# Performance work log

Hardware: AMD Instinct MI355X
Metric: run time of the kernel (lower is better)

## Reference

```python
import jax, jax.numpy as jnp
import numpy as np

DIM = 512
NUM_HEAD = 8
HEAD_DIM = DIM // NUM_HEAD
FFN = 4 * DIM


def setup_inputs() -> dict:
    key = jax.random.key(0)
    ks = jax.random.split(key, 16)
    s = DIM ** -0.5
    inp = {
        "x": jax.random.normal(ks[0], (4, 2048, DIM), jnp.float32),
        "wq": jax.random.normal(ks[1], (DIM, DIM), jnp.float32) * s,
        "bq": jnp.zeros((DIM,), jnp.float32),
        "wk": jax.random.normal(ks[2], (DIM, DIM), jnp.float32) * s,
        "bk": jnp.zeros((DIM,), jnp.float32),
        "wv": jax.random.normal(ks[3], (DIM, DIM), jnp.float32) * s,
        "bv": jnp.zeros((DIM,), jnp.float32),
        "wo": jax.random.normal(ks[4], (DIM, DIM), jnp.float32) * s,
        "bo": jnp.zeros((DIM,), jnp.float32),
        "w1": jax.random.normal(ks[5], (DIM, FFN), jnp.float32) * s,
        "b1": jnp.zeros((FFN,), jnp.float32),
        "w2": jax.random.normal(ks[6], (FFN, DIM), jnp.float32) * (FFN ** -0.5),
        "b2": jnp.zeros((DIM,), jnp.float32),
        "g1": jnp.ones((DIM,), jnp.float32),
        "be1": jnp.zeros((DIM,), jnp.float32),
        "g2": jnp.ones((DIM,), jnp.float32),
        "be2": jnp.zeros((DIM,), jnp.float32),
    }
    return inp


def layer_norm(x, g, b, eps=1e-5):
    mu = jnp.mean(x, axis=-1, keepdims=True)
    var = jnp.var(x, axis=-1, keepdims=True)
    return (x - mu) * jax.lax.rsqrt(var + eps) * g + b


def _forward(x, wq, bq, wk, bk, wv, bv, wo, bo, w1, b1, w2, b2, g1, be1, g2, be2):
    b, n, _ = x.shape
    scale = HEAD_DIM ** -0.5
    q = (x @ wq + bq).reshape(b, n, NUM_HEAD, HEAD_DIM).transpose(0, 2, 1, 3)
    k = (x @ wk + bk).reshape(b, n, NUM_HEAD, HEAD_DIM).transpose(0, 2, 1, 3)
    v = (x @ wv + bv).reshape(b, n, NUM_HEAD, HEAD_DIM).transpose(0, 2, 1, 3)
    scores = jnp.einsum('bhqd,bhkd->bhqk', q, k) * scale
    attn = jax.nn.softmax(scores, axis=-1)
    out = jnp.einsum('bhqk,bhkd->bhqd', attn, v)
    out = out.transpose(0, 2, 1, 3).reshape(b, n, DIM)
    out = out @ wo + bo
    x = layer_norm(out + x, g1, be1)
    h = jax.nn.gelu(x @ w1 + b1, approximate=False)
    ff = h @ w2 + b2
    x = layer_norm(ff + x, g2, be2)
    return x


def reference(x, wq, bq, wk, bk, wv, bv, wo, bo, w1, b1, w2, b2, g1, be1, g2, be2):
    return _forward(x, wq, bq, wk, bk, wv, bv, wo, bo, w1, b1, w2, b2, g1, be1, g2, be2)
```

## Files before the change

### kernel.cpp

```cpp
#include <hip/hip_runtime.h>
#include <math.h>

#define DIM 512
#define NHEAD 8
#define HD 64
#define FFN_DIM 2048
#define BATCH 4
#define SEQ 2048
#define MTOK (BATCH*SEQ)

typedef __attribute__((ext_vector_type(8))) short bf16x8;
typedef __attribute__((ext_vector_type(4))) short bf16x4;
typedef __attribute__((ext_vector_type(4))) float f32x4;
typedef __attribute__((ext_vector_type(2))) unsigned int u32x2;
typedef __attribute__((ext_vector_type(4))) unsigned int u32x4;

__device__ __forceinline__ unsigned short f2b(float f){
    unsigned int u = __float_as_uint(f);
    u += 0x7fffu + ((u >> 16) & 1u);
    return (unsigned short)(u >> 16);
}
__device__ __forceinline__ float b2f(unsigned short u){
    return __uint_as_float(((unsigned int)u) << 16);
}
__device__ __forceinline__ unsigned int pack_trunc(float f0, float f1){
    return __builtin_amdgcn_perm(__float_as_uint(f1), __float_as_uint(f0), 0x07060302u);
}
__device__ __forceinline__ void async_cp16(const unsigned short* g, unsigned short* l){
    __builtin_amdgcn_global_load_lds((const __attribute__((address_space(1))) unsigned int*)g,
                                     (__attribute__((address_space(3))) unsigned int*)l, 16, 0, 0);
}
__device__ __forceinline__ float gelu_fast(float x){
    float x3 = x*x*x;
    float y  = 2.302588f * (x + 0.044715f*x3);
    float t  = __builtin_amdgcn_exp2f(y);
    return x * t * __builtin_amdgcn_rcpf(t + 1.0f);
}

__device__ __forceinline__ void transp32(const float* __restrict__ in, unsigned short* __restrict__ out,
                                         int N, int K, int n0_rd, int n0_wr, int k0,
                                         unsigned short (&t)[32][33], int tid){
    int tx = tid & 31, ty = tid >> 5;
    #pragma unroll
    for (int u = 0; u < 4; u++)
        t[tx][ty + 8*u] = f2b(in[(size_t)(k0 + ty + 8*u)*N + n0_rd + tx]);
    __syncthreads();
    #pragma unroll
    for (int u = 0; u < 4; u++)
        out[(size_t)(n0_wr + ty + 8*u)*K + k0 + tx] = t[ty + 8*u][tx];
}

__global__ void prep_kernel(const float* __restrict__ x,
                            const float* __restrict__ wq, const float* __restrict__ wk,
                            const float* __restrict__ wv, const float* __restrict__ wo,
                            const float* __restrict__ w1, const float* __restrict__ w2,
                            const float* __restrict__ bq, const float* __restrict__ bk,
                            const float* __restrict__ bv,
                            unsigned short* __restrict__ xb, unsigned short* __restrict__ wqkvT,
                            unsigned short* __restrict__ woT, unsigned short* __restrict__ w1T,
                            unsigned short* __restrict__ w2T, float* __restrict__ bqkv)
{
    __shared__ unsigned short t[32][33];
    int bid = blockIdx.x, tid = threadIdx.x;
    if (bid < 4096) {
        int i = (bid*256 + tid)*4;
        float4 v = *(const float4*)(x + i);
        ushort4 o; o.x=f2b(v.x); o.y=f2b(v.y); o.z=f2b(v.z); o.w=f2b(v.w);
        *(ushort4*)(xb + i) = o;
    } else if (bid < 4864) {
        int r = bid - 4096;
        int n0 = (r % 48)*32, k0 = (r / 48)*32;
        const float* w = (n0 < 512) ? wq : (n0 < 1024) ? wk : wv;
        transp32(w, wqkvT, 512, 512, n0 & 511, n0, k0, t, tid);
    } else if (bid < 5120) {
        int r = bid - 4864;
        int n0 = (r % 16)*32, k0 = (r / 16)*32;
        transp32(wo, woT, 512, 512, n0, n0, k0, t, tid);
    } else if (bid < 6144) {
        int r = bid - 5120;
        int n0 = (r % 64)*32, k0 = (r / 64)*32;
        transp32(w1, w1T, 2048, 512, n0, n0, k0, t, tid);
    } else if (bid < 7168) {
        int r = bid - 6144;
        int n0 = (r % 16)*32, k0 = (r / 16)*32;
        transp32(w2, w2T, 512, 2048, n0, n0, k0, t, tid);
    } else {
        int i = (bid - 7168)*256 + tid;
        if (i < 1536)
            bqkv[i] = (i < 512) ? bq[i] : (i < 1024) ? bk[i-512] : bv[i-1024];
    }
}

template<int MODE, int SK>
__global__ __launch_bounds__(512, 4)
void gemm_bf16(const unsigned short* __restrict__ A, const unsigned short* __restrict__ Bt,
               const float* __restrict__ bias,
               unsigned short* __restrict__ Cb,
               unsigned short* __restrict__ qo, unsigned short* __restrict__ ko,
               unsigned short* __restrict__ vTo,
               int M, int N, int K)
{
    __shared__ unsigned short lds[36864];
    int tid  = threadIdx.x;
    int lane = tid & 63;
    int ln = lane & 15, qd = lane >> 4;
    int m0 = blockIdx.x * 256, n0 = blockIdx.y * 128;
    int wid = tid >> 6;
    int wm = (wid >> 1) * 64;
    int wn = (wid & 1) * 64;
    int kbeg = (SK > 1) ? (int)blockIdx.z * (K/SK) : 0;
    int nk = (K/SK) >> 5;
    if (SK > 1 && MODE == 0) Cb += (size_t)blockIdx.z * M * N;

    f32x4 acc[4][4];
    #pragma unroll
    for (int i = 0; i < 4; i++)
        #pragma unroll
        for (int j = 0; j < 4; j++) acc[i][j] = (f32x4){0.f,0.f,0.f,0.f};

#define G_STAGE(K0_, BUF_)                                                              \
    {                                                                                   \
        _Pragma("unroll")                                                               \
        for (int i = 0; i < 2; i++) {                                                   \
            int cid = i*512 + tid;                                                      \
            int row = cid >> 2, cs = cid & 3;                                           \
            int cg = cs ^ ((row >> 1) & 3);                                             \
            async_cp16(&A[(size_t)(m0+row)*K + (K0_) + cg*8], &lds[(BUF_) + (cid & ~63) * 8]); \
        }                                                                               \
        {                                                                               \
            int cid = tid;                                                              \
            int row = cid >> 2, cs = cid & 3;                                           \
            int cg = cs ^ ((row >> 1) & 3);                                             \
            async_cp16(&Bt[(size_t)(n0+row)*K + (K0_) + cg*8], &lds[(BUF_) + 8192 + (cid & ~63) * 8]); \
        }                                                                               \
    }

    G_STAGE(kbeg,      0)
    G_STAGE(kbeg + 32, 12288)

    int swz = (qd ^ ((ln >> 1) & 3)) * 8;
    int aoff = (wm + ln)*32 + swz;
    int boff = 8192 + (wn + ln)*32 + swz;

    int kof = 0;
    for (int t = 0; t < nk; t++) {
        if (t < nk - 1) { asm volatile("s_waitcnt vmcnt(3)" ::: "memory"); }
        else            { asm volatile("s_waitcnt vmcnt(0)" ::: "memory"); }
        __builtin_amdgcn_s_barrier();
        __builtin_amdgcn_sched_barrier(0);
        if (t < nk - 2) {
            int nb = kof + 24576; if (nb >= 36864) nb -= 36864;
            G_STAGE(kbeg + (t+2)*32, nb)
        }
        bf16x8 af[4], bf[4];
        #pragma unroll
        for (int tt = 0; tt < 4; tt++) {
            af[tt] = *(bf16x8*)&lds[kof + aoff + tt*512];
            bf[tt] = *(bf16x8*)&lds[kof + boff + tt*512];
        }
        __builtin_amdgcn_s_setprio(1);
        #pragma unroll
        for (int i = 0; i < 4; i++)
            #pragma unroll
            for (int j = 0; j < 4; j++)
                acc[i][j] = __builtin_amdgcn_mfma_f32_16x16x32_bf16(af[i], bf[j], acc[i][j], 0,0,0);
        __builtin_amdgcn_s_setprio(0);
        kof += 12288; if (kof >= 36864) kof = 0;
    }
#undef G_STAGE

    const float QSCALE = 0.18033688011112042f;
    #pragma unroll
    for (int i = 0; i < 4; i++) {
        int mb = m0 + wm + i*16 + qd*4;
        #pragma unroll
        for (int j = 0; j < 4; j++) {
            int c = n0 + wn + j*16 + ln;
            float bv_ = (SK > 1 && blockIdx.z) ? 0.f : bias[c];
            float v[4];
            #pragma unroll
            for (int r = 0; r < 4; r++) v[r] = acc[i][j][r] + bv_;
            if (MODE == 0) {
                #pragma unroll
                for (int r = 0; r < 4; r++) Cb[(size_t)(mb+r)*N + c] = f2b(v[r]);
            } else if (MODE == 2) {
                #pragma unroll
                for (int r = 0; r < 4; r++)
                    Cb[(size_t)(mb+r)*N + c] = f2b(gelu_fast(v[r]));
            } else {
                int b = mb >> 11, t0 = mb & 2047;
                if (c < 512) {
                    int h = c >> 6, hd = c & 63;
                    #pragma unroll
                    for (int r = 0; r < 4; r++)
                        qo[(((size_t)(b*8 + h))*SEQ + t0 + r)*64 + hd] = f2b(v[r] * QSCALE);
                } else if (c < 1024) {
                    int cc = c - 512, h = cc >> 6, hd = cc & 63;
                    #pragma unroll
                    for (int r = 0; r < 4; r++)
                        ko[(((size_t)(b*8 + h))*SEQ + t0 + r)*64 + hd] = f2b(v[r]);
                } else {
                    int cc = c - 1024, h = cc >> 6, hd = cc & 63;
                    ushort4 pk;
                    pk.x = f2b(v[0]); pk.y = f2b(v[1]); pk.z = f2b(v[2]); pk.w = f2b(v[3]);
                    *(ushort4*)&vTo[(((size_t)(b*8 + h))*64 + hd)*SEQ + t0] = pk;
                }
            }
        }
    }
}

#define ATTN_BODY(KT_, KOF_, PREF_, VMC_)                                               \
  {                                                                                     \
    asm volatile("s_waitcnt vmcnt(" #VMC_ ")" ::: "memory");                            \
    __builtin_amdgcn_s_barrier();                                                       \
    __builtin_amdgcn_sched_barrier(0);                                                  \
    if (PREF_) {                                                                        \
      const int nb = (KOF_ + 16384) % 24576;                                            \
      async_cp16(&K [((size_t)bh*SEQ + ((KT_)+2)*64 + srow)*64 + scg*8], &lds[nb + sdst]); \
      async_cp16(&VT[((size_t)bh*64 + srow)*SEQ + ((KT_)+2)*64 + scg*8], &lds[nb + 4096 + sdst]); \
    }                                                                                   \
    bf16x8 kf[2][2];                                                                    \
    _Pragma("unroll")                                                                   \
    for (int ntl = 0; ntl < 2; ntl++) {                                                 \
      kf[ntl][0] = *(const bf16x8*)&kp0[(KOF_) + ntl*1024];                             \
      kf[ntl][1] = *(const bf16x8*)&kp1[(KOF_) + ntl*1024];                             \
    }                                                                                   \
    f32x4 s[2][2];                                                                      \
    _Pragma("unroll")                                                                   \
    for (int qs = 0; qs < 2; qs++)                                                      \
      _Pragma("unroll")                                                                 \
      for (int ntl = 0; ntl < 2; ntl++) s[qs][ntl] = (f32x4){0.f,0.f,0.f,0.f};          \
    __builtin_amdgcn_s_setprio(1);                                                      \
    _Pragma("unroll")                                                                   \
    for (int kk = 0; kk < 2; kk++) {                                                    \
      _Pragma("unroll")                                                                 \
      for (int ntl = 0; ntl < 2; ntl++) {                                               \
        s[0][ntl] = __builtin_amdgcn_mfma_f32_16x16x32_bf16(kf[ntl][kk], qf[0][kk], s[0][ntl], 0,0,0); \
        s[1][ntl] = __builtin_amdgcn_mfma_f32_16x16x32_bf16(kf[ntl][kk], qf[1][kk], s[1][ntl], 0,0,0); \
      }                                                                                 \
    }                                                                                   \
    __builtin_amdgcn_s_setprio(0);                                                      \
    bf16x8 pf[2];                                                                       \
    _Pragma("unroll")                                                                   \
    for (int qs = 0; qs < 2; qs++) {                                                    \
      float p[8];                                                                       \
      _Pragma("unroll")                                                                 \
      for (int ntl = 0; ntl < 2; ntl++)                                                 \
        _Pragma("unroll")                                                               \
        for (int r = 0; r < 4; r++) p[ntl*4+r] = __builtin_amdgcn_exp2f(s[qs][ntl][r]); \
      l_i[qs] += ((p[0]+p[1])+(p[2]+p[3])) + ((p[4]+p[5])+(p[6]+p[7]));                 \
      u32x4 pu;                                                                         \
      pu[0] = pack_trunc(p[0], p[1]); pu[1] = pack_trunc(p[2], p[3]);                   \
      pu[2] = pack_trunc(p[4], p[5]); pu[3] = pack_trunc(p[6], p[7]);                   \
      pf[qs] = __builtin_bit_cast(bf16x8, pu);                                          \
    }                                                                                   \
    __builtin_amdgcn_s_setprio(1);                                                      \
    _Pragma("unroll")                                                                   \
    for (int dt = 0; dt < 4; dt++) {                                                    \
      u32x2 va = *(const u32x2*)&vpA[(KOF_) + 4096 + dt*1024];                          \
      u32x2 vb = *(const u32x2*)&vpB[(KOF_) + 4096 + dt*1024];                          \
      u32x4 vv; vv[0] = va[0]; vv[1] = va[1]; vv[2] = vb[0]; vv[3] = vb[1];             \
      bf16x8 vf = __builtin_bit_cast(bf16x8, vv);                                       \
      o[0][dt] = __builtin_amdgcn_mfma_f32_16x16x32_bf16(vf, pf[0], o[0][dt], 0,0,0);   \
      o[1][dt] = __builtin_amdgcn_mfma_f32_16x16x32_bf16(vf, pf[1], o[1][dt], 0,0,0);   \
    }                                                                                   \
    __builtin_amdgcn_s_setprio(0);                                                      \
  }

__global__ __launch_bounds__(512, 2)
void attn_mfma(const unsigned short* __restrict__ Q, const unsigned short* __restrict__ K,
               const unsigned short* __restrict__ VT, unsigned short* __restrict__ O)
{
    __shared__ unsigned short lds[24576];
    int tid  = threadIdx.x;
    int wid  = tid >> 6, lane = tid & 63;
    int ln = lane & 15, qd = lane >> 4;
    int wq = wid & 3;
    int wk = wid >> 2;
    int bx = blockIdx.x;
    int qb = (bx >> 3) & 15;
    int bh = (bx & 7) + 8 * (bx >> 7);

    bf16x8 qf[2][2];
    #pragma unroll
    for (int qs = 0; qs < 2; qs++)
        #pragma unroll
        for (int kk = 0; kk < 2; kk++)
            qf[qs][kk] = *(const bf16x8*)&Q[((size_t)bh*SEQ + qb*128 + wq*32 + qs*16 + ln)*64 + kk*32 + qd*8];

    int srow = tid >> 3, scs = tid & 7, scg = scs ^ (srow & 7);
    int sdst = (tid & ~63) * 8;
    #pragma unroll
    for (int t = 0; t < 2; t++) {
        async_cp16(&K [((size_t)bh*SEQ + t*64 + srow)*64 + scg*8], &lds[t*8192 + sdst]);
        async_cp16(&VT[((size_t)bh*64 + srow)*SEQ + t*64 + scg*8], &lds[t*8192 + 4096 + sdst]);
    }

    const unsigned short* kp0 = lds + wk*2048 + ln*64 + ((0*4 + qd) ^ (ln & 7))*8;
    const unsigned short* kp1 = lds + wk*2048 + ln*64 + ((1*4 + qd) ^ (ln & 7))*8;
    const unsigned short* vpA = lds + ln*64 + ((wk*4     + (qd>>1)) ^ (ln & 7))*8 + (qd & 1)*4;
    const unsigned short* vpB = lds + ln*64 + ((wk*4 + 2 + (qd>>1)) ^ (ln & 7))*8 + (qd & 1)*4;

    f32x4 o[2][4];
    #pragma unroll
    for (int qs = 0; qs < 2; qs++)
        #pragma unroll
        for (int dt = 0; dt < 4; dt++) o[qs][dt] = (f32x4){0.f,0.f,0.f,0.f};
    float l_i[2] = {0.f, 0.f};

    for (int kt3 = 0; kt3 < 30; kt3 += 3) {
        ATTN_BODY(kt3 + 0, 0,     true, 2)
        ATTN_BODY(kt3 + 1, 8192,  true, 2)
        ATTN_BODY(kt3 + 2, 16384, true, 2)
    }
    ATTN_BODY(30, 0,    false, 2)
    ATTN_BODY(31, 8192, false, 0)

    float l[2];
    #pragma unroll
    for (int qs = 0; qs < 2; qs++) {
        float t = l_i[qs];
        t += __shfl_xor(t, 16);
        t += __shfl_xor(t, 32);
        l[qs] = t;
    }

    __syncthreads();
    float* fl = (float*)lds;
    if (wk == 1) {
        #pragma unroll
        for (int qs = 0; qs < 2; qs++) {
            #pragma unroll
            for (int dt = 0; dt < 4; dt++)
                *(f32x4*)&fl[(((wq*2 + qs)*4 + dt)*64 + lane)*4] = o[qs][dt];
            fl[8192 + (wq*2 + qs)*64 + lane] = l[qs];
        }
    }
    __syncthreads();
    if (wk == 0) {
        int b = bh >> 3, h = bh & 7;
        #pragma unroll
        for (int qs = 0; qs < 2; qs++) {
            float lt = l[qs] + fl[8192 + (wq*2 + qs)*64 + lane];
            float linv = 1.0f / lt;
            int t = qb*128 + wq*32 + qs*16 + ln;
            #pragma unroll
            for (int dt = 0; dt < 4; dt++) {
                f32x4 po = *(f32x4*)&fl[(((wq*2 + qs)*4 + dt)*64 + lane)*4];
                ushort4 pk;
                pk.x = f2b((o[qs][dt][0] + po[0])*linv);
                pk.y = f2b((o[qs][dt][1] + po[1])*linv);
                pk.z = f2b((o[qs][dt][2] + po[2])*linv);
                pk.w = f2b((o[qs][dt][3] + po[3])*linv);
                *(ushort4*)&O[((size_t)b*SEQ + t)*DIM + h*64 + dt*16 + qd*4] = pk;
            }
        }
    }
}

__global__ void ln1_kernel(const unsigned short* __restrict__ m0b, const unsigned short* __restrict__ m1b,
                           const float* __restrict__ resp,
                           const float* __restrict__ g, const float* __restrict__ be,
                           unsigned short* __restrict__ outb)
{
    int row  = blockIdx.x*4 + (threadIdx.x >> 6);
    int lane = threadIdx.x & 63;
    size_t base = (size_t)row * DIM + lane*8;

    ushort4 a0 = *(const ushort4*)(m0b + base);
    ushort4 a1 = *(const ushort4*)(m0b + base + 4);
    ushort4 c0 = *(const ushort4*)(m1b + base);
    ushort4 c1 = *(const ushort4*)(m1b + base + 4);
    float4 r0 = *(const float4*)(resp + base);
    float4 r1 = *(const float4*)(resp + base + 4);
    float v[8] = { b2f(a0.x)+b2f(c0.x)+r0.x, b2f(a0.y)+b2f(c0.y)+r0.y,
                   b2f(a0.z)+b2f(c0.z)+r0.z, b2f(a0.w)+b2f(c0.w)+r0.w,
                   b2f(a1.x)+b2f(c1.x)+r1.x, b2f(a1.y)+b2f(c1.y)+r1.y,
                   b2f(a1.z)+b2f(c1.z)+r1.z, b2f(a1.w)+b2f(c1.w)+r1.w };
    float s = 0.f, s2 = 0.f;
    #pragma unroll
    for (int i = 0; i < 8; i++) { s += v[i]; s2 += v[i]*v[i]; }
    #pragma unroll
    for (int d = 32; d >= 1; d >>= 1) { s += __shfl_xor(s, d); s2 += __shfl_xor(s2, d); }
    float mean = s * (1.0f / DIM);
    float rstd = rsqrtf(s2 * (1.0f / DIM) - mean*mean + 1e-5f);

    float4 g0 = *(const float4*)(g + lane*8);
    float4 g1 = *(const float4*)(g + lane*8 + 4);
    float4 b0 = *(const float4*)(be + lane*8);
    float4 b1 = *(const float4*)(be + lane*8 + 4);
    float gg[8] = {g0.x,g0.y,g0.z,g0.w,g1.x,g1.y,g1.z,g1.w};
    float bb[8] = {b0.x,b0.y,b0.z,b0.w,b1.x,b1.y,b1.z,b1.w};
    float o[8];
    #pragma unroll
    for (int i = 0; i < 8; i++) o[i] = (v[i]-mean)*rstd*gg[i] + bb[i];
    ushort4 p0, p1;
    p0.x=f2b(o[0]); p0.y=f2b(o[1]); p0.z=f2b(o[2]); p0.w=f2b(o[3]);
    p1.x=f2b(o[4]); p1.y=f2b(o[5]); p1.z=f2b(o[6]); p1.w=f2b(o[7]);
    *(ushort4*)(outb + base)     = p0;
    *(ushort4*)(outb + base + 4) = p1;
}

__global__ void ln2_kernel(const unsigned short* __restrict__ m0b, const unsigned short* __restrict__ m1b,
                           const unsigned short* __restrict__ resb,
                           const float* __restrict__ g, const float* __restrict__ be,
                           float* __restrict__ outf)
{
    int row  = blockIdx.x*4 + (threadIdx.x >> 6);
    int lane = threadIdx.x & 63;
    size_t base = (size_t)row * DIM + lane*8;

    ushort4 a0 = *(const ushort4*)(m0b + base);
    ushort4 a1 = *(const ushort4*)(m0b + base + 4);
    ushort4 c0 = *(const ushort4*)(m1b + base);
    ushort4 c1 = *(const ushort4*)(m1b + base + 4);
    ushort4 rb0 = *(const ushort4*)(resb + base);
    ushort4 rb1 = *(const ushort4*)(resb + base + 4);
    float v[8] = { b2f(a0.x)+b2f(c0.x)+b2f(rb0.x), b2f(a0.y)+b2f(c0.y)+b2f(rb0.y),
                   b2f(a0.z)+b2f(c0.z)+b2f(rb0.z), b2f(a0.w)+b2f(c0.w)+b2f(rb0.w),
                   b2f(a1.x)+b2f(c1.x)+b2f(rb1.x), b2f(a1.y)+b2f(c1.y)+b2f(rb1.y),
                   b2f(a1.z)+b2f(c1.z)+b2f(rb1.z), b2f(a1.w)+b2f(c1.w)+b2f(rb1.w) };
    float s = 0.f, s2 = 0.f;
    #pragma unroll
    for (int i = 0; i < 8; i++) { s += v[i]; s2 += v[i]*v[i]; }
    #pragma unroll
    for (int d = 32; d >= 1; d >>= 1) { s += __shfl_xor(s, d); s2 += __shfl_xor(s2, d); }
    float mean = s * (1.0f / DIM);
    float rstd = rsqrtf(s2 * (1.0f / DIM) - mean*mean + 1e-5f);

    float4 g0 = *(const float4*)(g + lane*8);
    float4 g1 = *(const float4*)(g + lane*8 + 4);
    float4 b0 = *(const float4*)(be + lane*8);
    float4 b1 = *(const float4*)(be + lane*8 + 4);
    float gg[8] = {g0.x,g0.y,g0.z,g0.w,g1.x,g1.y,g1.z,g1.w};
    float bb[8] = {b0.x,b0.y,b0.z,b0.w,b1.x,b1.y,b1.z,b1.w};
    float o[8];
    #pragma unroll
    for (int i = 0; i < 8; i++) o[i] = (v[i] - mean)*rstd*gg[i] + bb[i];
    *(float4*)(outf + base)     = (float4){o[0],o[1],o[2],o[3]};
    *(float4*)(outf + base + 4) = (float4){o[4],o[5],o[6],o[7]};
}

extern "C" void kernel_launch(void* const* d_in, const int* in_sizes, int n_in,
                              void* d_out, int out_size, void* d_ws, size_t ws_size,
                              hipStream_t stream) {
    const float* x   = (const float*)d_in[0];
    const float* wq  = (const float*)d_in[1];
    const float* bq  = (const float*)d_in[2];
    const float* wk  = (const float*)d_in[3];
    const float* bk  = (const float*)d_in[4];
    const float* wv  = (const float*)d_in[5];
    const float* bv  = (const float*)d_in[6];
    const float* wo  = (const float*)d_in[7];
    const float* bo  = (const float*)d_in[8];
    const float* w1  = (const float*)d_in[9];
    const float* b1  = (const float*)d_in[10];
    const float* w2  = (const float*)d_in[11];
    const float* b2  = (const float*)d_in[12];
    const float* g1  = (const float*)d_in[13];
    const float* be1 = (const float*)d_in[14];
    const float* g2  = (const float*)d_in[15];
    const float* be2 = (const float*)d_in[16];
    float* out = (float*)d_out;

    char* w = (char*)d_ws;
    size_t off = 0;
    auto alloc = [&](size_t bytes){ void* p = w + off; off += (bytes + 255) & ~(size_t)255; return p; };
    unsigned short* xb     = (unsigned short*)alloc((size_t)MTOK*DIM*2);
    unsigned short* wqkvT  = (unsigned short*)alloc((size_t)1536*512*2);
    unsigned short* woT    = (unsigned short*)alloc((size_t)512*512*2);
    unsigned short* w1T    = (unsigned short*)alloc((size_t)2048*512*2);
    unsigned short* w2T    = (unsigned short*)alloc((size_t)512*2048*2);
    float*          bqkv   = (float*)alloc(1536*4);
    unsigned short* qb_    = (unsigned short*)alloc((size_t)32*SEQ*64*2);
    unsigned short* kb_    = (unsigned short*)alloc((size_t)32*SEQ*64*2);
    unsigned short* vT_    = (unsigned short*)alloc((size_t)32*64*SEQ*2);
    unsigned short* attno  = (unsigned short*)alloc((size_t)MTOK*DIM*2);
    unsigned short* x1b    = (unsigned short*)alloc((size_t)MTOK*DIM*2);
    unsigned short* h_     = (unsigned short*)alloc((size_t)MTOK*FFN_DIM*2);
    unsigned short* ffb    = (unsigned short*)alloc((size_t)2*MTOK*DIM*2);

    prep_kernel<<<7174, 256, 0, stream>>>(x, wq, wk, wv, wo, w1, w2, bq, bk, bv,
                                          xb, wqkvT, woT, w1T, w2T, bqkv);

    gemm_bf16<1,1><<<dim3(32,12), 512, 0, stream>>>(xb, wqkvT, bqkv, nullptr,
                                                    qb_, kb_, vT_, MTOK, 1536, DIM);
    attn_mfma<<<512, 512, 0, stream>>>(qb_, kb_, vT_, attno);
    gemm_bf16<0,2><<<dim3(32,4,2), 512, 0, stream>>>(attno, woT, bo, ffb,
                                                     nullptr, nullptr, nullptr, MTOK, DIM, DIM);
    ln1_kernel<<<MTOK/4, 256, 0, stream>>>(ffb, ffb + (size_t)MTOK*DIM, x, g1, be1, x1b);
    gemm_bf16<2,1><<<dim3(32,16), 512, 0, stream>>>(x1b, w1T, b1, h_,
                                                    nullptr, nullptr, nullptr, MTOK, FFN_DIM, DIM);
    gemm_bf16<0,2><<<dim3(32,4,2), 512, 0, stream>>>(h_, w2T, b2, ffb,
                                                     nullptr, nullptr, nullptr, MTOK, DIM, FFN_DIM);
    ln2_kernel<<<MTOK/4, 256, 0, stream>>>(ffb, ffb + (size_t)MTOK*DIM, x1b, g2, be2, out);
}
```

Before: 238.9 us.

## Software-pipeline attention QK^T one tile ahead with 4-stage LDS ring

Restructures the attention inner loop so that each iteration computes QK^T scores for the next key tile while it runs exp/PV on the current tile, ping-ponging between two score register sets. The K/V shared-memory ring grows from three to four 8K-element stages with prefetch distance three, so loads are issued further ahead. This aims to overlap MFMA latency of the two matmuls and hide global-load latency. In exchange it uses more registers and more LDS per block, which may reduce occupancy at the requested launch bounds of 2 blocks.

```diff
diff --git a/kernel.cpp b/kernel.cpp
--- a/kernel.cpp
+++ b/kernel.cpp
@@ -210,37 +210,37 @@
     }
 }
 
-#define ATTN_BODY(KT_, KOF_, PREF_, VMC_)                                               \
+#define ATTN_ITER(T_, VBUF_, K1BUF_, PBUF_, PREF_, VMC_, SC_, SN_, DOQK_)               \
   {                                                                                     \
     asm volatile("s_waitcnt vmcnt(" #VMC_ ")" ::: "memory");                            \
     __builtin_amdgcn_s_barrier();                                                       \
     __builtin_amdgcn_sched_barrier(0);                                                  \
     if (PREF_) {                                                                        \
-      const int nb = (KOF_ + 16384) % 24576;                                            \
-      async_cp16(&K [((size_t)bh*SEQ + ((KT_)+2)*64 + srow)*64 + scg*8], &lds[nb + sdst]); \
-      async_cp16(&VT[((size_t)bh*64 + srow)*SEQ + ((KT_)+2)*64 + scg*8], &lds[nb + 4096 + sdst]); \
+      async_cp16(&K [((size_t)bh*SEQ + ((T_)+3)*64 + srow)*64 + scg*8], &lds[(PBUF_) + sdst]); \
+      async_cp16(&VT[((size_t)bh*64 + srow)*SEQ + ((T_)+3)*64 + scg*8], &lds[(PBUF_) + 4096 + sdst]); \
     }                                                                                   \
-    bf16x8 kf[2][2];                                                                    \
-    _Pragma("unroll")                                                                   \
-    for (int ntl = 0; ntl < 2; ntl++) {                                                 \
-      kf[ntl][0] = *(const bf16x8*)&kp0[(KOF_) + ntl*1024];                             \
-      kf[ntl][1] = *(const bf16x8*)&kp1[(KOF_) + ntl*1024];                             \
-    }                                                                                   \
-    f32x4 s[2][2];                                                                      \
-    _Pragma("unroll")                                                                   \
-    for (int qs = 0; qs < 2; qs++)                                                      \
-      _Pragma("unroll")                                                                 \
-      for (int ntl = 0; ntl < 2; ntl++) s[qs][ntl] = (f32x4){0.f,0.f,0.f,0.f};          \
-    __builtin_amdgcn_s_setprio(1);                                                      \
-    _Pragma("unroll")                                                                   \
-    for (int kk = 0; kk < 2; kk++) {                                                    \
+    if (DOQK_) {                                                                        \
+      bf16x8 kf[2][2];                                                                  \
       _Pragma("unroll")                                                                 \
       for (int ntl = 0; ntl < 2; ntl++) {                                               \
-        s[0][ntl] = __builtin_amdgcn_mfma_f32_16x16x32_bf16(kf[ntl][kk], qf[0][kk], s[0][ntl], 0,0,0); \
-        s[1][ntl] = __builtin_amdgcn_mfma_f32_16x16x32_bf16(kf[ntl][kk], qf[1][kk], s[1][ntl], 0,0,0); \
+        kf[ntl][0] = *(const bf16x8*)&kp0[(K1BUF_) + ntl*1024];                         \
+        kf[ntl][1] = *(const bf16x8*)&kp1[(K1BUF_) + ntl*1024];                         \
       }                                                                                 \
+      _Pragma("unroll")                                                                 \
+      for (int qs = 0; qs < 2; qs++)                                                    \
+        _Pragma("unroll")                                                               \
+        for (int ntl = 0; ntl < 2; ntl++) SN_[qs][ntl] = (f32x4){0.f,0.f,0.f,0.f};      \
+      __builtin_amdgcn_s_setprio(1);                                                    \
+      _Pragma("unroll")                                                                 \
+      for (int kk = 0; kk < 2; kk++) {                                                  \
+        _Pragma("unroll")                                                               \
+        for (int ntl = 0; ntl < 2; ntl++) {                                             \
+          SN_[0][ntl] = __builtin_amdgcn_mfma_f32_16x16x32_bf16(kf[ntl][kk], qf[0][kk], SN_[0][ntl], 0,0,0); \
+          SN_[1][ntl] = __builtin_amdgcn_mfma_f32_16x16x32_bf16(kf[ntl][kk], qf[1][kk], SN_[1][ntl], 0,0,0); \
+        }                                                                               \
+      }                                                                                 \
+      __builtin_amdgcn_s_setprio(0);                                                    \
     }                                                                                   \
-    __builtin_amdgcn_s_setprio(0);                                                      \
     bf16x8 pf[2];                                                                       \
     _Pragma("unroll")                                                                   \
     for (int qs = 0; qs < 2; qs++) {                                                    \
@@ -248,7 +248,7 @@
       _Pragma("unroll")                                                                 \
       for (int ntl = 0; ntl < 2; ntl++)                                                 \
         _Pragma("unroll")                                                               \
-        for (int r = 0; r < 4; r++) p[ntl*4+r] = __builtin_amdgcn_exp2f(s[qs][ntl][r]); \
+        for (int r = 0; r < 4; r++) p[ntl*4+r] = __builtin_amdgcn_exp2f(SC_[qs][ntl][r]); \
       l_i[qs] += ((p[0]+p[1])+(p[2]+p[3])) + ((p[4]+p[5])+(p[6]+p[7]));                 \
       u32x4 pu;                                                                         \
       pu[0] = pack_trunc(p[0], p[1]); pu[1] = pack_trunc(p[2], p[3]);                   \
@@ -258,8 +258,8 @@
     __builtin_amdgcn_s_setprio(1);                                                      \
     _Pragma("unroll")                                                                   \
     for (int dt = 0; dt < 4; dt++) {                                                    \
-      u32x2 va = *(const u32x2*)&vpA[(KOF_) + 4096 + dt*1024];                          \
-      u32x2 vb = *(const u32x2*)&vpB[(KOF_) + 4096 + dt*1024];                          \
+      u32x2 va = *(const u32x2*)&vpA[(VBUF_) + 4096 + dt*1024];                         \
+      u32x2 vb = *(const u32x2*)&vpB[(VBUF_) + 4096 + dt*1024];                         \
       u32x4 vv; vv[0] = va[0]; vv[1] = va[1]; vv[2] = vb[0]; vv[3] = vb[1];             \
       bf16x8 vf = __builtin_bit_cast(bf16x8, vv);                                       \
       o[0][dt] = __builtin_amdgcn_mfma_f32_16x16x32_bf16(vf, pf[0], o[0][dt], 0,0,0);   \
@@ -272,7 +272,7 @@
 void attn_mfma(const unsigned short* __restrict__ Q, const unsigned short* __restrict__ K,
                const unsigned short* __restrict__ VT, unsigned short* __restrict__ O)
 {
-    __shared__ unsigned short lds[24576];
+    __shared__ unsigned short lds[32768];
     int tid  = threadIdx.x;
     int wid  = tid >> 6, lane = tid & 63;
     int ln = lane & 15, qd = lane >> 4;
@@ -292,7 +292,7 @@
     int srow = tid >> 3, scs = tid & 7, scg = scs ^ (srow & 7);
     int sdst = (tid & ~63) * 8;
     #pragma unroll
-    for (int t = 0; t < 2; t++) {
+    for (int t = 0; t < 3; t++) {
         async_cp16(&K [((size_t)bh*SEQ + t*64 + srow)*64 + scg*8], &lds[t*8192 + sdst]);
         async_cp16(&VT[((size_t)bh*64 + srow)*SEQ + t*64 + scg*8], &lds[t*8192 + 4096 + sdst]);
     }
@@ -308,14 +308,42 @@
         #pragma unroll
         for (int dt = 0; dt < 4; dt++) o[qs][dt] = (f32x4){0.f,0.f,0.f,0.f};
     float l_i[2] = {0.f, 0.f};
-
-    for (int kt3 = 0; kt3 < 30; kt3 += 3) {
-        ATTN_BODY(kt3 + 0, 0,     true, 2)
-        ATTN_BODY(kt3 + 1, 8192,  true, 2)
-        ATTN_BODY(kt3 + 2, 16384, true, 2)
-    }
-    ATTN_BODY(30, 0,    false, 2)
-    ATTN_BODY(31, 8192, false, 0)
+    f32x4 sA[2][2], sB[2][2];
+
+    asm volatile("s_waitcnt vmcnt(4)" ::: "memory");
+    __builtin_amdgcn_s_barrier();
+    __builtin_amdgcn_sched_barrier(0);
+    {
+        bf16x8 kf[2][2];
+        #pragma unroll
+        for (int ntl = 0; ntl < 2; ntl++) {
+            kf[ntl][0] = *(const bf16x8*)&kp0[ntl*1024];
+            kf[ntl][1] = *(const bf16x8*)&kp1[ntl*1024];
+        }
+        #pragma unroll
+        for (int qs = 0; qs < 2; qs++)
+            #pragma unroll
+            for (int ntl = 0; ntl < 2; ntl++) sA[qs][ntl] = (f32x4){0.f,0.f,0.f,0.f};
+        #pragma unroll
+        for (int kk = 0; kk < 2; kk++) {
+            #pragma unroll
+            for (int ntl = 0; ntl < 2; ntl++) {
+                sA[0][ntl] = __builtin_amdgcn_mfma_f32_16x16x32_bf16(kf[ntl][kk], qf[0][kk], sA[0][ntl], 0,0,0);
+                sA[1][ntl] = __builtin_amdgcn_mfma_f32_16x16x32_bf16(kf[ntl][kk], qf[1][kk], sA[1][ntl], 0,0,0);
+            }
+        }
+    }
+
+    for (int t4 = 0; t4 < 28; t4 += 4) {
+        ATTN_ITER(t4+0, 0,     8192,  24576, true, 2, sA, sB, true)
+        ATTN_ITER(t4+1, 8192,  16384, 0,     true, 2, sB, sA, true)
+        ATTN_ITER(t4+2, 16384, 24576, 8192,  true, 2, sA, sB, true)
+        ATTN_ITER(t4+3, 24576, 0,     16384, true, 2, sB, sA, true)
+    }
+    ATTN_ITER(28, 0,     8192,  24576, true,  2, sA, sB, true)
+    ATTN_ITER(29, 8192,  16384, 0,     false, 2, sB, sA, true)
+    ATTN_ITER(30, 16384, 24576, 0,     false, 0, sA, sB, true)
+    ATTN_ITER(31, 24576, 0,     0,     false, 0, sB, sA, false)
 
     float l[2];
     #pragma unroll
```

Measured after the change: 240.7 us. No clear change (+0.8%).

## Split attention over two key halves and merge partials in a combine kernel

Applied to the files above, without the earlier changes.

The attention grid gains a second dimension, so each block processes only half of the key sequence (16 tiles instead of 32). Each block writes unnormalized partial outputs in bf16 plus per-row softmax denominators. A new combine kernel adds the two partials and divides by the summed denominators. This doubles the block count to raise parallelism and shorten each block's serial key loop. In exchange it adds a second launch, extra global traffic for the partial outputs, a duplicated pipeline prologue per block, and rounding of unnormalized partials to bf16.

```diff
diff --git a/kernel.cpp b/kernel.cpp
--- a/kernel.cpp
+++ b/kernel.cpp
@@ -217,8 +217,8 @@
     __builtin_amdgcn_sched_barrier(0);                                                  \
     if (PREF_) {                                                                        \
       const int nb = (KOF_ + 16384) % 24576;                                            \
-      async_cp16(&K [((size_t)bh*SEQ + ((KT_)+2)*64 + srow)*64 + scg*8], &lds[nb + sdst]); \
-      async_cp16(&VT[((size_t)bh*64 + srow)*SEQ + ((KT_)+2)*64 + scg*8], &lds[nb + 4096 + sdst]); \
+      async_cp16(&K [((size_t)bh*SEQ + (kzo+(KT_)+2)*64 + srow)*64 + scg*8], &lds[nb + sdst]); \
+      async_cp16(&VT[((size_t)bh*64 + srow)*SEQ + (kzo+(KT_)+2)*64 + scg*8], &lds[nb + 4096 + sdst]); \
     }                                                                                   \
     bf16x8 kf[2][2];                                                                    \
     _Pragma("unroll")                                                                   \
@@ -270,7 +270,9 @@
 
 __global__ __launch_bounds__(512, 2)
 void attn_mfma(const unsigned short* __restrict__ Q, const unsigned short* __restrict__ K,
-               const unsigned short* __restrict__ VT, unsigned short* __restrict__ O)
+               const unsigned short* __restrict__ VT,
+               unsigned short* __restrict__ O0, unsigned short* __restrict__ O1,
+               float* __restrict__ LP)
 {
     __shared__ unsigned short lds[24576];
     int tid  = threadIdx.x;
@@ -281,6 +283,8 @@
     int bx = blockIdx.x;
     int qb = (bx >> 3) & 15;
     int bh = (bx & 7) + 8 * (bx >> 7);
+    int kz = blockIdx.y;
+    int kzo = kz << 4;
 
     bf16x8 qf[2][2];
     #pragma unroll
@@ -293,8 +297,8 @@
     int sdst = (tid & ~63) * 8;
     #pragma unroll
     for (int t = 0; t < 2; t++) {
-        async_cp16(&K [((size_t)bh*SEQ + t*64 + srow)*64 + scg*8], &lds[t*8192 + sdst]);
-        async_cp16(&VT[((size_t)bh*64 + srow)*SEQ + t*64 + scg*8], &lds[t*8192 + 4096 + sdst]);
+        async_cp16(&K [((size_t)bh*SEQ + (kzo+t)*64 + srow)*64 + scg*8], &lds[t*8192 + sdst]);
+        async_cp16(&VT[((size_t)bh*64 + srow)*SEQ + (kzo+t)*64 + scg*8], &lds[t*8192 + 4096 + sdst]);
     }
 
     const unsigned short* kp0 = lds + wk*2048 + ln*64 + ((0*4 + qd) ^ (ln & 7))*8;
@@ -309,13 +313,15 @@
         for (int dt = 0; dt < 4; dt++) o[qs][dt] = (f32x4){0.f,0.f,0.f,0.f};
     float l_i[2] = {0.f, 0.f};
 
-    for (int kt3 = 0; kt3 < 30; kt3 += 3) {
+    for (int kt3 = 0; kt3 < 12; kt3 += 3) {
         ATTN_BODY(kt3 + 0, 0,     true, 2)
         ATTN_BODY(kt3 + 1, 8192,  true, 2)
         ATTN_BODY(kt3 + 2, 16384, true, 2)
     }
-    ATTN_BODY(30, 0,    false, 2)
-    ATTN_BODY(31, 8192, false, 0)
+    ATTN_BODY(12, 0,     true,  2)
+    ATTN_BODY(13, 8192,  true,  2)
+    ATTN_BODY(14, 16384, false, 2)
+    ATTN_BODY(15, 0,     false, 0)
 
     float l[2];
     #pragma unroll
@@ -340,23 +346,53 @@
     __syncthreads();
     if (wk == 0) {
         int b = bh >> 3, h = bh & 7;
+        unsigned short* op = kz ? O1 : O0;
+        float* lp = LP + (size_t)kz * 32 * SEQ;
         #pragma unroll
         for (int qs = 0; qs < 2; qs++) {
             float lt = l[qs] + fl[8192 + (wq*2 + qs)*64 + lane];
-            float linv = 1.0f / lt;
             int t = qb*128 + wq*32 + qs*16 + ln;
+            if (qd == 0) lp[(size_t)bh*SEQ + t] = lt;
             #pragma unroll
             for (int dt = 0; dt < 4; dt++) {
                 f32x4 po = *(f32x4*)&fl[(((wq*2 + qs)*4 + dt)*64 + lane)*4];
                 ushort4 pk;
-                pk.x = f2b((o[qs][dt][0] + po[0])*linv);
-                pk.y = f2b((o[qs][dt][1] + po[1])*linv);
-                pk.z = f2b((o[qs][dt][2] + po[2])*linv);
-                pk.w = f2b((o[qs][dt][3] + po[3])*linv);
-                *(ushort4*)&O[((size_t)b*SEQ + t)*DIM + h*64 + dt*16 + qd*4] = pk;
+                pk.x = f2b(o[qs][dt][0] + po[0]);
+                pk.y = f2b(o[qs][dt][1] + po[1]);
+                pk.z = f2b(o[qs][dt][2] + po[2]);
+                pk.w = f2b(o[qs][dt][3] + po[3]);
+                *(ushort4*)&op[((size_t)b*SEQ + t)*DIM + h*64 + dt*16 + qd*4] = pk;
             }
         }
     }
+}
+
+__global__ void attn_combine(const unsigned short* __restrict__ o0p, const unsigned short* __restrict__ o1p,
+                             const float* __restrict__ l0p, const float* __restrict__ l1p,
+                             unsigned short* __restrict__ outb)
+{
+    int row  = blockIdx.x*4 + (threadIdx.x >> 6);
+    int lane = threadIdx.x & 63;
+    int b = row >> 11, t = row & 2047;
+    int h = lane >> 3;
+    int li = (b*8 + h)*SEQ + t;
+    float linv = 1.0f / (l0p[li] + l1p[li]);
+    size_t base = (size_t)row * DIM + lane*8;
+    ushort4 a0 = *(const ushort4*)(o0p + base);
+    ushort4 a1 = *(const ushort4*)(o0p + base + 4);
+    ushort4 c0 = *(const ushort4*)(o1p + base);
+    ushort4 c1 = *(const ushort4*)(o1p + base + 4);
+    ushort4 p0, p1;
+    p0.x = f2b((b2f(a0.x)+b2f(c0.x))*linv);
+    p0.y = f2b((b2f(a0.y)+b2f(c0.y))*linv);
+    p0.z = f2b((b2f(a0.z)+b2f(c0.z))*linv);
+    p0.w = f2b((b2f(a0.w)+b2f(c0.w))*linv);
+    p1.x = f2b((b2f(a1.x)+b2f(c1.x))*linv);
+    p1.y = f2b((b2f(a1.y)+b2f(c1.y))*linv);
+    p1.z = f2b((b2f(a1.z)+b2f(c1.z))*linv);
+    p1.w = f2b((b2f(a1.w)+b2f(c1.w))*linv);
+    *(ushort4*)(outb + base)     = p0;
+    *(ushort4*)(outb + base + 4) = p1;
 }
 
 __global__ void ln1_kernel(const unsigned short* __restrict__ m0b, const unsigned short* __restrict__ m1b,
@@ -477,6 +513,8 @@
     unsigned short* kb_    = (unsigned short*)alloc((size_t)32*SEQ*64*2);
     unsigned short* vT_    = (unsigned short*)alloc((size_t)32*64*SEQ*2);
     unsigned short* attno  = (unsigned short*)alloc((size_t)MTOK*DIM*2);
+    unsigned short* op1    = (unsigned short*)alloc((size_t)MTOK*DIM*2);
+    float*          lp_    = (float*)alloc((size_t)2*32*SEQ*4);
     unsigned short* x1b    = (unsigned short*)alloc((size_t)MTOK*DIM*2);
     unsigned short* h_     = (unsigned short*)alloc((size_t)MTOK*FFN_DIM*2);
     unsigned short* ffb    = (unsigned short*)alloc((size_t)2*MTOK*DIM*2);
@@ -486,7 +524,8 @@
 
     gemm_bf16<1,1><<<dim3(32,12), 512, 0, stream>>>(xb, wqkvT, bqkv, nullptr,
                                                     qb_, kb_, vT_, MTOK, 1536, DIM);
-    attn_mfma<<<512, 512, 0, stream>>>(qb_, kb_, vT_, attno);
+    attn_mfma<<<dim3(512,2), 512, 0, stream>>>(qb_, kb_, vT_, attno, op1, lp_);
+    attn_combine<<<MTOK/4, 256, 0, stream>>>(attno, op1, lp_, lp_ + (size_t)32*SEQ, attno);
     gemm_bf16<0,2><<<dim3(32,4,2), 512, 0, stream>>>(attno, woT, bo, ffb,
                                                      nullptr, nullptr, nullptr, MTOK, DIM, DIM);
     ln1_kernel<<<MTOK/4, 256, 0, stream>>>(ffb, ffb + (size_t)MTOK*DIM, x, g1, be1, x1b);
```

Result: slower. 246.4 us (+3.1%).
